# Kernel tuning notes

Hardware: AMD Instinct MI355X
Metric: run time of the kernel (lower is better)

Reference implementation:

```python
import jax, jax.numpy as jnp
from jax import lax
import numpy as np

B, CIN, HC, K, REC = 64, 64, 64, 3, 5
MG = 240 // REC  # 48
EPS = 1e-8


def conv2d(x, w, b, pad):
    y = lax.conv_general_dilated(x, w, (1, 1), [(pad, pad), (pad, pad)],
                                 dimension_numbers=('NCHW', 'OIHW', 'NCHW'))
    return y + b[None, :, None, None]


def conv_transpose2d(x, w, b, stride, pad):
    # PyTorch ConvTranspose2d: w is (Cin, Cout, kH, kW)
    k = w.shape[2]
    w_t = jnp.transpose(w[:, :, ::-1, ::-1], (1, 0, 2, 3))  # -> OIHW, flipped
    y = lax.conv_general_dilated(x, w_t, (1, 1),
                                 [(k - 1 - pad, k - 1 - pad)] * 2,
                                 lhs_dilation=(stride, stride),
                                 dimension_numbers=('NCHW', 'OIHW', 'NCHW'))
    return y + b[None, :, None, None]


def leaky(x):
    return jnp.where(x >= 0, x, 0.2 * x)


def setup_inputs() -> dict:
    key = jax.random.key(0)
    ks = jax.random.split(key, 12)
    s = 0.05
    return {
        'x': jax.random.normal(ks[0], (B, CIN, 64, 64), jnp.float32),
        'h': jax.random.normal(ks[1], (B, HC, 64, 64), jnp.float32),
        'c': jax.random.normal(ks[2], (B, HC, 64, 64), jnp.float32),
        'recalled_memory_feature': jax.random.normal(ks[3], (B, REC, MG, 32, 32), jnp.float32),
        'conv_w': jax.random.normal(ks[4], (5 * HC, CIN + HC, K, K), jnp.float32) * s,
        'conv_b': jax.random.normal(ks[5], (5 * HC,), jnp.float32) * s,
        'convc_w': jax.random.normal(ks[6], (MG, HC, 1, 1), jnp.float32) * s,
        'convc_b': jax.random.normal(ks[7], (MG,), jnp.float32) * s,
        'convssm_w': jax.random.normal(ks[8], (MG, MG, 4, 4), jnp.float32) * s,
        'convssm_b': jax.random.normal(ks[9], (MG,), jnp.float32) * s,
        'convfuse_w': jax.random.normal(ks[10], (HC, MG + HC, 1, 1), jnp.float32) * s,
        'convfuse_b': jax.random.normal(ks[11], (HC,), jnp.float32) * s,
    }


def reference(x, h, c, recalled_memory_feature, conv_w, conv_b, convc_w, convc_b,
              convssm_w, convssm_b, convfuse_w, convfuse_b):
    rm = recalled_memory_feature.reshape(B, REC, MG, 32, 32)
    rm_avg = rm.mean(axis=(3, 4))                      # (B, REC, MG)
    q = leaky(conv2d(c, convc_w, convc_b, 0))          # (B, MG, 64, 64)
    q_avg = q.mean(axis=(2, 3))                        # (B, MG)
    # cosine similarity along channel dim, vectorized over (B, REC)
    qn = jnp.maximum(jnp.linalg.norm(q_avg, axis=1, keepdims=True), EPS)   # (B,1)
    mn = jnp.maximum(jnp.linalg.norm(rm_avg, axis=2), EPS)                  # (B,REC)
    cos = jnp.einsum('bm,brm->br', q_avg, rm_avg) / (qn * mn)               # (B,REC)
    attn = jax.nn.softmax(cos, axis=1)                                      # (B,REC)
    mt = jnp.einsum('br,brmhw->bmhw', attn, rm)        # (B, MG, 32, 32)
    mt = leaky(conv_transpose2d(mt, convssm_w, convssm_b, 2, 1))  # (B, MG, 64, 64)

    gates = conv2d(jnp.concatenate((x, h), axis=1), conv_w, conv_b, K // 2)
    i, f, g, o, lam = jnp.split(gates, 5, axis=1)
    i = jax.nn.sigmoid(i)
    f = jax.nn.sigmoid(f)
    o = jax.nn.sigmoid(o)
    g = jnp.tanh(g)
    lam = jax.nn.sigmoid(lam)
    c_new = f * c + i * g
    h_new = o * jnp.tanh(conv2d(jnp.concatenate((c_new, mt), axis=1), convfuse_w, convfuse_b, 0))
    h_out = lam * h_new + (1.0 - lam) * h
    return (h_out, c_new)
```

## Files before the change

### kernel.cpp

```cpp
#include <hip/hip_runtime.h>
#include <hip/hip_bf16.h>
#include <cstdint>

#define HW 4096
#define MGc 48
#define RECc 5

typedef __attribute__((ext_vector_type(8))) short bf16x8;
typedef __attribute__((ext_vector_type(4))) float f32x4;

__device__ __forceinline__ float sigf(float x) { return 1.f / (1.f + expf(-x)); }
__device__ __forceinline__ float leakyf(float x) { return x >= 0.f ? x : 0.2f * x; }
__device__ __forceinline__ unsigned short f2bfu(float f) {
  __hip_bfloat16 b = __float2bfloat16(f);
  return *reinterpret_cast<unsigned short*>(&b);
}
__device__ __forceinline__ float bfu2f(unsigned short u) {
  unsigned v = ((unsigned)u) << 16;
  return __uint_as_float(v);
}
__device__ __forceinline__ void gload_lds16(const void* g, void* l) {
  __builtin_amdgcn_global_load_lds(
      (const __attribute__((address_space(1))) unsigned int*)g,
      (__attribute__((address_space(3))) unsigned int*)l, 16, 0, 0);
}

__global__ __launch_bounds__(256) void k_prep(const float* __restrict__ cw,
    __hip_bfloat16* __restrict__ Wp, __hip_bfloat16* __restrict__ Pp) {
  if (blockIdx.x < 1440) {
    int idx = blockIdx.x * 256 + threadIdx.x;
    int t = idx / (320 * 128);
    int rem = idx % (320 * 128);
    int ocp = rem / 128, ci = rem % 128;
    int nt = ocp / 80, r2 = ocp % 80, gate = r2 / 16, ml = r2 % 16;
    int oc = gate * 64 + nt * 16 + ml;
    Wp[idx] = __float2bfloat16(cw[((size_t)oc * 128 + ci) * 9 + t]);
  } else {
    int idx = (blockIdx.x - 1440) * 256 + threadIdx.x;
    int b = idx / 4160, i = idx % 4160;
    bf16x8* base = reinterpret_cast<bf16x8*>(Pp);
    size_t u;
    if (i < 2112) {
      int r = (i < 1056) ? 0 : 65;
      int j = (i < 1056) ? i : i - 1056;
      u = ((size_t)b * 66 + r) * 1056 + j;
    } else {
      int i2 = i - 2112;
      int row = 1 + (i2 >> 5), k = i2 & 31;
      int px = (k < 16) ? 0 : 65, ci8 = k & 15;
      u = (((size_t)b * 66 + row) * 66 + px) * 16 + ci8;
    }
    base[u] = (bf16x8)0;
  }
}

__global__ __launch_bounds__(256) void k_rm_sum(const float* __restrict__ rm,
                                                float* __restrict__ rm_sum) {
  int row = blockIdx.x;
  const float4* p = reinterpret_cast<const float4*>(rm + (size_t)row * 1024);
  float4 v = p[threadIdx.x];
  float s = v.x + v.y + v.z + v.w;
  #pragma unroll
  for (int off = 32; off; off >>= 1) s += __shfl_down(s, off);
  __shared__ float sred[4];
  if ((threadIdx.x & 63) == 0) sred[threadIdx.x >> 6] = s;
  __syncthreads();
  if (threadIdx.x == 0) rm_sum[row] = sred[0] + sred[1] + sred[2] + sred[3];
}

__global__ __launch_bounds__(256) void k_q_part(const float* __restrict__ c,
    const float* __restrict__ ccw, const float* __restrict__ ccb,
    float* __restrict__ q_part) {
  __shared__ float wl[MGc * 64];
  __shared__ float bl[MGc];
  __shared__ float red[4][MGc];
  int b = blockIdx.y, seg = blockIdx.x;
  for (int i = threadIdx.x; i < MGc * 64; i += 256) wl[i] = ccw[i];
  if (threadIdx.x < MGc) bl[threadIdx.x] = ccb[threadIdx.x];
  __syncthreads();
  int px = seg * 256 + threadIdx.x;
  float acc[MGc];
  #pragma unroll
  for (int m = 0; m < MGc; m++) acc[m] = 0.f;
  const float* cp = c + (size_t)b * 64 * HW + px;
  for (int ci = 0; ci < 64; ci++) {
    float v = cp[(size_t)ci * HW];
    #pragma unroll
    for (int m = 0; m < MGc; m++) acc[m] += wl[m * 64 + ci] * v;
  }
  int lane = threadIdx.x & 63, wv = threadIdx.x >> 6;
  #pragma unroll
  for (int m = 0; m < MGc; m++) {
    float t = leakyf(acc[m] + bl[m]);
    #pragma unroll
    for (int off = 32; off; off >>= 1) t += __shfl_down(t, off);
    if (lane == 0) red[wv][m] = t;
  }
  __syncthreads();
  if (threadIdx.x < MGc) {
    float t = red[0][threadIdx.x] + red[1][threadIdx.x] + red[2][threadIdx.x] + red[3][threadIdx.x];
    q_part[((size_t)b * 16 + seg) * MGc + threadIdx.x] = t;
  }
}

__global__ __launch_bounds__(256) void k_mt_pre(const float* __restrict__ rm,
    const float* __restrict__ rm_sum, const float* __restrict__ q_part,
    float* __restrict__ mt_pre) {
  __shared__ float sat[RECc];
  int idx = blockIdx.x * 256 + threadIdx.x;
  int b = idx / (MGc * 1024);
  if (threadIdx.x < 64) {
    int lane = threadIdx.x;
    float q = 0.f;
    if (lane < MGc) {
      float s = 0.f;
      for (int sg = 0; sg < 16; sg++) s += q_part[((size_t)b * 16 + sg) * MGc + lane];
      q = s * (1.f / 4096.f);
    }
    float qs = q * q;
    #pragma unroll
    for (int off = 32; off; off >>= 1) qs += __shfl_xor(qs, off);
    float qn = fmaxf(sqrtf(qs), 1e-8f);
    float cosv[RECc];
    #pragma unroll
    for (int r = 0; r < RECc; r++) {
      float m = 0.f;
      if (lane < MGc) m = rm_sum[((size_t)b * RECc + r) * MGc + lane] * (1.f / 1024.f);
      float d = q * m, ms = m * m;
      #pragma unroll
      for (int off = 32; off; off >>= 1) { d += __shfl_xor(d, off); ms += __shfl_xor(ms, off); }
      float mn = fmaxf(sqrtf(ms), 1e-8f);
      cosv[r] = d / (qn * mn);
    }
    float mx = cosv[0];
    #pragma unroll
    for (int r = 1; r < RECc; r++) mx = fmaxf(mx, cosv[r]);
    float ssum = 0.f;
    #pragma unroll
    for (int r = 0; r < RECc; r++) { cosv[r] = expf(cosv[r] - mx); ssum += cosv[r]; }
    float inv = 1.f / ssum;
    #pragma unroll
    for (int r = 0; r < RECc; r++)
      if (lane == r) sat[r] = cosv[r] * inv;
  }
  __syncthreads();
  int rem = idx - b * (MGc * 1024);
  const float* base = rm + (size_t)b * RECc * MGc * 1024 + rem;
  float v = sat[0] * base[0] + sat[1] * base[MGc * 1024] + sat[2] * base[2 * MGc * 1024]
          + sat[3] * base[3 * MGc * 1024] + sat[4] * base[4 * MGc * 1024];
  mt_pre[idx] = v;
}

__global__ __launch_bounds__(512) void k_ssm(const float* __restrict__ mt_pre,
    const float* __restrict__ w, const float* __restrict__ bias,
    __hip_bfloat16* __restrict__ mt) {
  __shared__ float in_t[12][10][20];
  __shared__ float w_t[12][48][16];
  int b = blockIdx.y;
  int tile = blockIdx.x;
  int y0 = (tile >> 1) * 16, x0 = (tile & 1) * 32;
  int wv = threadIdx.x >> 6, lane = threadIdx.x & 63;
  int co0 = wv * 6;
  int oyl = lane >> 2, xseg = lane & 3;
  int oy = y0 + oyl;
  int iy0 = (y0 >> 1) - 1, ix0 = (x0 >> 1) - 1;
  int kyA = (oy + 1) & 1;
  int iyA = (oy + 1 - kyA) >> 1;
  int rA = iyA - iy0, rB = rA - 1;
  float acc[6][8] = {};
  for (int ch = 0; ch < 4; ch++) {
    int ci0 = ch * 12;
    __syncthreads();
    for (int i = threadIdx.x; i < 12 * 10 * 18; i += 512) {
      int ci = i / 180, rr = (i % 180) / 18, cc2 = i % 18;
      int giy = iy0 + rr, gix = ix0 + cc2;
      float v = 0.f;
      if ((unsigned)giy < 32u && (unsigned)gix < 32u)
        v = mt_pre[(((size_t)b * MGc + ci0 + ci) * 32 + giy) * 32 + gix];
      in_t[ci][rr][cc2] = v;
    }
    for (int i = threadIdx.x; i < 12 * 48 * 16; i += 512)
      (&w_t[0][0][0])[i] = w[ci0 * 768 + i];
    __syncthreads();
    #pragma unroll 1
    for (int ci = 0; ci < 12; ci++) {
      float4 a0 = *reinterpret_cast<const float4*>(&in_t[ci][rA][xseg * 4]);
      float4 a1 = *reinterpret_cast<const float4*>(&in_t[ci][rA][xseg * 4 + 4]);
      float4 b0 = *reinterpret_cast<const float4*>(&in_t[ci][rB][xseg * 4]);
      float4 b1 = *reinterpret_cast<const float4*>(&in_t[ci][rB][xseg * 4 + 4]);
      float vA[6] = {a0.x, a0.y, a0.z, a0.w, a1.x, a1.y};
      float vB[6] = {b0.x, b0.y, b0.z, b0.w, b1.x, b1.y};
      #pragma unroll
      for (int co = 0; co < 6; co++) {
        const float* wp = &w_t[ci][co0 + co][0];
        float4 wA = *reinterpret_cast<const float4*>(wp + kyA * 4);
        float4 wB = *reinterpret_cast<const float4*>(wp + (kyA + 2) * 4);
        #pragma unroll
        for (int j = 0; j < 8; j++) {
          if ((j & 1) == 0) {
            int hi = (j >> 1) + 1, lo = j >> 1;
            acc[co][j] += vA[hi] * wA.y + vA[lo] * wA.w + vB[hi] * wB.y + vB[lo] * wB.w;
          } else {
            int hi = ((j + 1) >> 1) + 1, lo = (j + 1) >> 1;
            acc[co][j] += vA[hi] * wA.x + vA[lo] * wA.z + vB[hi] * wB.x + vB[lo] * wB.z;
          }
        }
      }
    }
  }
  int oxb = x0 + xseg * 8;
  #pragma unroll
  for (int co = 0; co < 6; co++) {
    float bb = bias[co0 + co];
    size_t obase = (((size_t)b * MGc + co0 + co) * 64 + oy) * 64 + oxb;
    #pragma unroll
    for (int j = 0; j < 8; j++)
      mt[obase + j] = __float2bfloat16(leakyf(acc[co][j] + bb));
  }
}

__global__ __launch_bounds__(256) void k_ppack(const float* __restrict__ xin,
    const float* __restrict__ hin, __hip_bfloat16* __restrict__ Pp) {
  __shared__ float t[64][65];
  int b = blockIdx.z, y = blockIdx.y, half = blockIdx.x;
  const float* src = (half ? hin : xin) + (size_t)b * 64 * HW + y * 64;
  #pragma unroll
  for (int it = 0; it < 4; it++) {
    int li = it * 256 + threadIdx.x;
    int ci = li >> 4, x4 = (li & 15) * 4;
    float4 v = *reinterpret_cast<const float4*>(src + (size_t)ci * HW + x4);
    t[x4][ci] = v.x; t[x4 + 1][ci] = v.y; t[x4 + 2][ci] = v.z; t[x4 + 3][ci] = v.w;
  }
  __syncthreads();
  int x = threadIdx.x >> 2, c16 = (threadIdx.x & 3) * 16;
  unsigned short* dst = reinterpret_cast<unsigned short*>(Pp) +
      ((((size_t)b * 66 + y + 1) * 66 + x + 1) * 128 + half * 64 + c16);
  bf16x8 o0, o1;
  #pragma unroll
  for (int j = 0; j < 8; j++) {
    o0[j] = (short)f2bfu(t[x][c16 + j]);
    o1[j] = (short)f2bfu(t[x][c16 + 8 + j]);
  }
  *reinterpret_cast<bf16x8*>(dst) = o0;
  *reinterpret_cast<bf16x8*>(dst + 8) = o1;
}

__global__ __launch_bounds__(256) void k_gates_mfma(
    const __hip_bfloat16* __restrict__ Pp, const __hip_bfloat16* __restrict__ Wp,
    const float* __restrict__ c, const float* __restrict__ cb,
    float* __restrict__ c_new, __hip_bfloat16* __restrict__ o_g,
    __hip_bfloat16* __restrict__ lam_g) {
  __shared__ bf16x8 s_in[18 * 4 * 18];
  __shared__ bf16x8 s_w[9 * 4 * 80];
  int orig = blockIdx.y * gridDim.x + blockIdx.x;
  int t_id = (orig & 7) * 512 + (orig >> 3);
  int b = t_id >> 6;
  int r6 = t_id & 63;
  int ytile = r6 >> 4, xtile = (r6 >> 2) & 3, nt = r6 & 3;
  int y0 = ytile * 16, x0 = xtile * 16;
  int tid = threadIdx.x;
  int wv = tid >> 6, lane = tid & 63;
  int lane15 = lane & 15, lq = lane >> 4;

  f32x4 acc[4][5];
  #pragma unroll
  for (int i = 0; i < 4; i++)
    #pragma unroll
    for (int j = 0; j < 5; j++) acc[i][j] = (f32x4)0.f;

  const char* Pb = (const char*)Pp;
  const char* Wb = (const char*)Wp;

  #pragma unroll 1
  for (int cc = 0; cc < 4; cc++) {
    __syncthreads();
    #pragma unroll 1
    for (int u = wv; u < 21; u += 4) {
      int e = u * 64 + lane;
      if (e < 1296) {
        int L = e / 72, r = e - L * 72;
        int llq = r / 18, xi = r - llq * 18;
        const char* gp = Pb + ((((size_t)b * 66 + y0 + L) * 66 + (x0 + xi)) * 256)
                         + cc * 64 + llq * 16;
        gload_lds16(gp, (void*)&s_in[e]);
      }
    }
    #pragma unroll 1
    for (int u = wv; u < 45; u += 4) {
      int e = u * 64 + lane;
      int unit = e / 80, ol = e - unit * 80;
      int t = unit >> 2, g = unit & 3;
      const char* gp = Wb + (((size_t)t * 320 + nt * 80 + ol) * 128 + cc * 32 + g * 8) * 2;
      gload_lds16(gp, (void*)&s_w[e]);
    }
    __syncthreads();

    #pragma unroll
    for (int dx = 0; dx < 3; dx++) {
      #pragma unroll
      for (int ky = 0; ky < 3; ky++) {
        int t = ky * 3 + dx;
        bf16x8 af[4];
        #pragma unroll
        for (int rr = 0; rr < 4; rr++)
          af[rr] = s_in[((wv * 4 + rr + ky) * 4 + lq) * 18 + lane15 + dx];
        bf16x8 bw[5];
        #pragma unroll
        for (int gg = 0; gg < 5; gg++)
          bw[gg] = s_w[(t * 4 + lq) * 80 + gg * 16 + lane15];
        __builtin_amdgcn_s_setprio(1);
        #pragma unroll
        for (int rr = 0; rr < 4; rr++)
          #pragma unroll
          for (int gg = 0; gg < 5; gg++)
            acc[rr][gg] = __builtin_amdgcn_mfma_f32_16x16x32_bf16(
                af[rr], bw[gg], acc[rr][gg], 0, 0, 0);
        __builtin_amdgcn_s_setprio(0);
      }
    }
  }

  int m_hid = nt * 16 + lane15;
  float bi = cb[m_hid], bff = cb[64 + m_hid], bgg = cb[128 + m_hid],
        bo = cb[192 + m_hid], bl = cb[256 + m_hid];
  int xb = x0 + lq * 4;
  size_t chofs = ((size_t)b * 64 + m_hid) * HW;
  #pragma unroll
  for (int rr = 0; rr < 4; rr++) {
    int y = y0 + wv * 4 + rr;
    size_t pofs = chofs + (size_t)y * 64 + xb;
    f32x4 cold = *reinterpret_cast<const f32x4*>(c + pofs);
    f32x4 cn;
    unsigned short ov[4], lv[4];
    #pragma unroll
    for (int e = 0; e < 4; e++) {
      float i_ = sigf(acc[rr][0][e] + bi);
      float f_ = sigf(acc[rr][1][e] + bff);
      float g_ = tanhf(acc[rr][2][e] + bgg);
      float o_ = sigf(acc[rr][3][e] + bo);
      float l_ = sigf(acc[rr][4][e] + bl);
      cn[e] = f_ * cold[e] + i_ * g_;
      ov[e] = f2bfu(o_);
      lv[e] = f2bfu(l_);
    }
    *reinterpret_cast<f32x4*>(c_new + pofs) = cn;
    ushort4 ovv = {ov[0], ov[1], ov[2], ov[3]};
    ushort4 lvv = {lv[0], lv[1], lv[2], lv[3]};
    *reinterpret_cast<ushort4*>(reinterpret_cast<unsigned short*>(o_g) + pofs) = ovv;
    *reinterpret_cast<ushort4*>(reinterpret_cast<unsigned short*>(lam_g) + pofs) = lvv;
  }
}

__global__ __launch_bounds__(256) void k_fuse(const float* __restrict__ c_new,
    const __hip_bfloat16* __restrict__ mt, const __hip_bfloat16* __restrict__ o_g,
    const __hip_bfloat16* __restrict__ lam_g, const float* __restrict__ h,
    const float* __restrict__ fw, const float* __restrict__ fb,
    float* __restrict__ h_out) {
  __shared__ float wl[112][64];
  int b = blockIdx.y, seg = blockIdx.x;
  for (int i = threadIdx.x; i < 112 * 64; i += 256) {
    int ci = i >> 6, co = i & 63;
    wl[ci][co] = fw[co * 112 + ci];
  }
  __syncthreads();
  int px = seg * 512 + threadIdx.x * 2;
  size_t bofs = (size_t)b * 64 * HW;
  float2 acc[64];
  #pragma unroll
  for (int co = 0; co < 64; co++) { float bv = fb[co]; acc[co].x = bv; acc[co].y = bv; }
  #pragma unroll 1
  for (int ci = 0; ci < 64; ci++) {
    float2 v = *reinterpret_cast<const float2*>(c_new + bofs + (size_t)ci * HW + px);
    #pragma unroll
    for (int c4 = 0; c4 < 16; c4++) {
      float4 w = *reinterpret_cast<const float4*>(&wl[ci][c4 * 4]);
      acc[c4 * 4 + 0].x += w.x * v.x; acc[c4 * 4 + 0].y += w.x * v.y;
      acc[c4 * 4 + 1].x += w.y * v.x; acc[c4 * 4 + 1].y += w.y * v.y;
      acc[c4 * 4 + 2].x += w.z * v.x; acc[c4 * 4 + 2].y += w.z * v.y;
      acc[c4 * 4 + 3].x += w.w * v.x; acc[c4 * 4 + 3].y += w.w * v.y;
    }
  }
  const unsigned short* mtu = reinterpret_cast<const unsigned short*>(mt);
  size_t mtofs = (size_t)b * MGc * HW + px;
  #pragma unroll 1
  for (int ci = 0; ci < 48; ci++) {
    unsigned u = *reinterpret_cast<const unsigned*>(mtu + mtofs + (size_t)ci * HW);
    float vx = bfu2f((unsigned short)(u & 0xffff));
    float vy = bfu2f((unsigned short)(u >> 16));
    #pragma unroll
    for (int c4 = 0; c4 < 16; c4++) {
      float4 w = *reinterpret_cast<const float4*>(&wl[64 + ci][c4 * 4]);
      acc[c4 * 4 + 0].x += w.x * vx; acc[c4 * 4 + 0].y += w.x * vy;
      acc[c4 * 4 + 1].x += w.y * vx; acc[c4 * 4 + 1].y += w.y * vy;
      acc[c4 * 4 + 2].x += w.z * vx; acc[c4 * 4 + 2].y += w.z * vy;
      acc[c4 * 4 + 3].x += w.w * vx; acc[c4 * 4 + 3].y += w.w * vy;
    }
  }
  const unsigned short* ou = reinterpret_cast<const unsigned short*>(o_g);
  const unsigned short* lu = reinterpret_cast<const unsigned short*>(lam_g);
  #pragma unroll
  for (int co = 0; co < 64; co++) {
    size_t ofs = bofs + (size_t)co * HW + px;
    unsigned uo = *reinterpret_cast<const unsigned*>(ou + ofs);
    unsigned ul = *reinterpret_cast<const unsigned*>(lu + ofs);
    float2 hv = *reinterpret_cast<const float2*>(h + ofs);
    float hnx = tanhf(acc[co].x), hny = tanhf(acc[co].y);
    float ox = bfu2f((unsigned short)(uo & 0xffff)), oy = bfu2f((unsigned short)(uo >> 16));
    float lx = bfu2f((unsigned short)(ul & 0xffff)), ly = bfu2f((unsigned short)(ul >> 16));
    float2 r;
    r.x = lx * (ox * hnx) + (1.f - lx) * hv.x;
    r.y = ly * (oy * hny) + (1.f - ly) * hv.y;
    *reinterpret_cast<float2*>(h_out + ofs) = r;
  }
}

extern "C" void kernel_launch(void* const* d_in, const int* in_sizes, int n_in,
                              void* d_out, int out_size, void* d_ws, size_t ws_size,
                              hipStream_t stream) {
  const float* x   = (const float*)d_in[0];
  const float* h   = (const float*)d_in[1];
  const float* c   = (const float*)d_in[2];
  const float* rm  = (const float*)d_in[3];
  const float* cw  = (const float*)d_in[4];
  const float* cb  = (const float*)d_in[5];
  const float* ccw = (const float*)d_in[6];
  const float* ccb = (const float*)d_in[7];
  const float* sw  = (const float*)d_in[8];
  const float* sb  = (const float*)d_in[9];
  const float* fw  = (const float*)d_in[10];
  const float* fb  = (const float*)d_in[11];

  float* h_out = (float*)d_out;
  float* c_new = h_out + (size_t)16777216;

  char* ws = (char*)d_ws;
  float* rm_sum = (float*)(ws + 0);
  float* q_part = (float*)(ws + 65536);
  float* mt_pre = (float*)(ws + 262144);
  __hip_bfloat16* o_g   = (__hip_bfloat16*)(ws + 0);
  __hip_bfloat16* lam_g = (__hip_bfloat16*)(ws + 33554432);
  __hip_bfloat16* mt    = (__hip_bfloat16*)(ws + 67108864);
  __hip_bfloat16* Pp    = (__hip_bfloat16*)(ws + 92274688);
  __hip_bfloat16* Wp    = (__hip_bfloat16*)(ws + 163643392);

  k_prep<<<2480, 256, 0, stream>>>(cw, Wp, Pp);
  k_ppack<<<dim3(2, 64, 64), 256, 0, stream>>>(x, h, Pp);
  k_rm_sum<<<15360, 256, 0, stream>>>(rm, rm_sum);
  k_q_part<<<dim3(16, 64), 256, 0, stream>>>(c, ccw, ccb, q_part);
  k_mt_pre<<<12288, 256, 0, stream>>>(rm, rm_sum, q_part, mt_pre);
  k_ssm<<<dim3(8, 64), 512, 0, stream>>>(mt_pre, sw, sb, mt);
  k_gates_mfma<<<dim3(64, 64), 256, 0, stream>>>(Pp, Wp, c, cb, c_new, o_g, lam_g);
  k_fuse<<<dim3(8, 64), 256, 0, stream>>>(c_new, mt, o_g, lam_g, h, fw, fb, h_out);
}
```

Before: 637.1 us.

## Merge four prologue kernels into one launch and hoist gate-kernel load addressing

Four independent prologue kernels (weight prep and padding zeroing, input packing, memory row sums, query partial sums) are merged into one launch that dispatches on block index, cutting launch count and letting the phases overlap on the GPU. In the gates MFMA kernel, the global-to-LDS copy addresses are computed once before the channel-chunk loop instead of in every iteration. The A-fragment loads from LDS are also restructured so six rows are loaded once per dx and reused across the three ky taps. The merged kernel reserves the largest shared-memory footprint for every block, which can lower occupancy for the small-footprint branches. The gates kernel now holds more registers for the precomputed pointers and extra fragments.

```diff
diff --git a/kernel.cpp b/kernel.cpp
--- a/kernel.cpp
+++ b/kernel.cpp
@@ -25,18 +25,25 @@
       (__attribute__((address_space(3))) unsigned int*)l, 16, 0, 0);
 }
 
-__global__ __launch_bounds__(256) void k_prep(const float* __restrict__ cw,
-    __hip_bfloat16* __restrict__ Wp, __hip_bfloat16* __restrict__ Pp) {
-  if (blockIdx.x < 1440) {
-    int idx = blockIdx.x * 256 + threadIdx.x;
+__global__ __launch_bounds__(256) void k_head(const float* __restrict__ cw,
+    __hip_bfloat16* __restrict__ Wp, __hip_bfloat16* __restrict__ Pp,
+    const float* __restrict__ xin, const float* __restrict__ hin,
+    const float* __restrict__ rm, float* __restrict__ rm_sum,
+    const float* __restrict__ c, const float* __restrict__ ccw,
+    const float* __restrict__ ccb, float* __restrict__ q_part) {
+  __shared__ __align__(16) char smem[16704];
+  int bid = blockIdx.x;
+  int tid = threadIdx.x;
+  if (bid < 1440) {
+    int idx = bid * 256 + tid;
     int t = idx / (320 * 128);
     int rem = idx % (320 * 128);
     int ocp = rem / 128, ci = rem % 128;
     int nt = ocp / 80, r2 = ocp % 80, gate = r2 / 16, ml = r2 % 16;
     int oc = gate * 64 + nt * 16 + ml;
     Wp[idx] = __float2bfloat16(cw[((size_t)oc * 128 + ci) * 9 + t]);
-  } else {
-    int idx = (blockIdx.x - 1440) * 256 + threadIdx.x;
+  } else if (bid < 2480) {
+    int idx = (bid - 1440) * 256 + tid;
     int b = idx / 4160, i = idx % 4160;
     bf16x8* base = reinterpret_cast<bf16x8*>(Pp);
     size_t u;
@@ -51,55 +58,73 @@
       u = (((size_t)b * 66 + row) * 66 + px) * 16 + ci8;
     }
     base[u] = (bf16x8)0;
-  }
-}
-
-__global__ __launch_bounds__(256) void k_rm_sum(const float* __restrict__ rm,
-                                                float* __restrict__ rm_sum) {
-  int row = blockIdx.x;
-  const float4* p = reinterpret_cast<const float4*>(rm + (size_t)row * 1024);
-  float4 v = p[threadIdx.x];
-  float s = v.x + v.y + v.z + v.w;
-  #pragma unroll
-  for (int off = 32; off; off >>= 1) s += __shfl_down(s, off);
-  __shared__ float sred[4];
-  if ((threadIdx.x & 63) == 0) sred[threadIdx.x >> 6] = s;
-  __syncthreads();
-  if (threadIdx.x == 0) rm_sum[row] = sred[0] + sred[1] + sred[2] + sred[3];
-}
-
-__global__ __launch_bounds__(256) void k_q_part(const float* __restrict__ c,
-    const float* __restrict__ ccw, const float* __restrict__ ccb,
-    float* __restrict__ q_part) {
-  __shared__ float wl[MGc * 64];
-  __shared__ float bl[MGc];
-  __shared__ float red[4][MGc];
-  int b = blockIdx.y, seg = blockIdx.x;
-  for (int i = threadIdx.x; i < MGc * 64; i += 256) wl[i] = ccw[i];
-  if (threadIdx.x < MGc) bl[threadIdx.x] = ccb[threadIdx.x];
-  __syncthreads();
-  int px = seg * 256 + threadIdx.x;
-  float acc[MGc];
-  #pragma unroll
-  for (int m = 0; m < MGc; m++) acc[m] = 0.f;
-  const float* cp = c + (size_t)b * 64 * HW + px;
-  for (int ci = 0; ci < 64; ci++) {
-    float v = cp[(size_t)ci * HW];
-    #pragma unroll
-    for (int m = 0; m < MGc; m++) acc[m] += wl[m * 64 + ci] * v;
-  }
-  int lane = threadIdx.x & 63, wv = threadIdx.x >> 6;
-  #pragma unroll
-  for (int m = 0; m < MGc; m++) {
-    float t = leakyf(acc[m] + bl[m]);
-    #pragma unroll
-    for (int off = 32; off; off >>= 1) t += __shfl_down(t, off);
-    if (lane == 0) red[wv][m] = t;
-  }
-  __syncthreads();
-  if (threadIdx.x < MGc) {
-    float t = red[0][threadIdx.x] + red[1][threadIdx.x] + red[2][threadIdx.x] + red[3][threadIdx.x];
-    q_part[((size_t)b * 16 + seg) * MGc + threadIdx.x] = t;
+  } else if (bid < 10672) {
+    float (*t)[65] = (float(*)[65])smem;
+    int r = bid - 2480;
+    int half = r & 1, y = (r >> 1) & 63, b = r >> 7;
+    const float* src = (half ? hin : xin) + (size_t)b * 64 * HW + y * 64;
+    #pragma unroll
+    for (int it = 0; it < 4; it++) {
+      int li = it * 256 + tid;
+      int ci = li >> 4, x4 = (li & 15) * 4;
+      float4 v = *reinterpret_cast<const float4*>(src + (size_t)ci * HW + x4);
+      t[x4][ci] = v.x; t[x4 + 1][ci] = v.y; t[x4 + 2][ci] = v.z; t[x4 + 3][ci] = v.w;
+    }
+    __syncthreads();
+    int x = tid >> 2, c16 = (tid & 3) * 16;
+    unsigned short* dst = reinterpret_cast<unsigned short*>(Pp) +
+        ((((size_t)b * 66 + y + 1) * 66 + x + 1) * 128 + half * 64 + c16);
+    bf16x8 o0, o1;
+    #pragma unroll
+    for (int j = 0; j < 8; j++) {
+      o0[j] = (short)f2bfu(t[x][c16 + j]);
+      o1[j] = (short)f2bfu(t[x][c16 + 8 + j]);
+    }
+    *reinterpret_cast<bf16x8*>(dst) = o0;
+    *reinterpret_cast<bf16x8*>(dst + 8) = o1;
+  } else if (bid < 26032) {
+    float* sred = (float*)smem;
+    int row = bid - 10672;
+    const float4* p = reinterpret_cast<const float4*>(rm + (size_t)row * 1024);
+    float4 v = p[tid];
+    float s = v.x + v.y + v.z + v.w;
+    #pragma unroll
+    for (int off = 32; off; off >>= 1) s += __shfl_down(s, off);
+    if ((tid & 63) == 0) sred[tid >> 6] = s;
+    __syncthreads();
+    if (tid == 0) rm_sum[row] = sred[0] + sred[1] + sred[2] + sred[3];
+  } else {
+    float* wl = (float*)smem;
+    float* bl = wl + MGc * 64;
+    float (*red)[MGc] = (float(*)[MGc])(bl + 64);
+    int r = bid - 26032;
+    int seg = r & 15, b = r >> 4;
+    for (int i = tid; i < MGc * 64; i += 256) wl[i] = ccw[i];
+    if (tid < MGc) bl[tid] = ccb[tid];
+    __syncthreads();
+    int px = seg * 256 + tid;
+    float acc[MGc];
+    #pragma unroll
+    for (int m = 0; m < MGc; m++) acc[m] = 0.f;
+    const float* cp = c + (size_t)b * 64 * HW + px;
+    for (int ci = 0; ci < 64; ci++) {
+      float v = cp[(size_t)ci * HW];
+      #pragma unroll
+      for (int m = 0; m < MGc; m++) acc[m] += wl[m * 64 + ci] * v;
+    }
+    int lane = tid & 63, wv = tid >> 6;
+    #pragma unroll
+    for (int m = 0; m < MGc; m++) {
+      float t2 = leakyf(acc[m] + bl[m]);
+      #pragma unroll
+      for (int off = 32; off; off >>= 1) t2 += __shfl_down(t2, off);
+      if (lane == 0) red[wv][m] = t2;
+    }
+    __syncthreads();
+    if (tid < MGc) {
+      float t2 = red[0][tid] + red[1][tid] + red[2][tid] + red[3][tid];
+      q_part[((size_t)b * 16 + seg) * MGc + tid] = t2;
+    }
   }
 }
 
@@ -219,32 +244,6 @@
   }
 }
 
-__global__ __launch_bounds__(256) void k_ppack(const float* __restrict__ xin,
-    const float* __restrict__ hin, __hip_bfloat16* __restrict__ Pp) {
-  __shared__ float t[64][65];
-  int b = blockIdx.z, y = blockIdx.y, half = blockIdx.x;
-  const float* src = (half ? hin : xin) + (size_t)b * 64 * HW + y * 64;
-  #pragma unroll
-  for (int it = 0; it < 4; it++) {
-    int li = it * 256 + threadIdx.x;
-    int ci = li >> 4, x4 = (li & 15) * 4;
-    float4 v = *reinterpret_cast<const float4*>(src + (size_t)ci * HW + x4);
-    t[x4][ci] = v.x; t[x4 + 1][ci] = v.y; t[x4 + 2][ci] = v.z; t[x4 + 3][ci] = v.w;
-  }
-  __syncthreads();
-  int x = threadIdx.x >> 2, c16 = (threadIdx.x & 3) * 16;
-  unsigned short* dst = reinterpret_cast<unsigned short*>(Pp) +
-      ((((size_t)b * 66 + y + 1) * 66 + x + 1) * 128 + half * 64 + c16);
-  bf16x8 o0, o1;
-  #pragma unroll
-  for (int j = 0; j < 8; j++) {
-    o0[j] = (short)f2bfu(t[x][c16 + j]);
-    o1[j] = (short)f2bfu(t[x][c16 + 8 + j]);
-  }
-  *reinterpret_cast<bf16x8*>(dst) = o0;
-  *reinterpret_cast<bf16x8*>(dst + 8) = o1;
-}
-
 __global__ __launch_bounds__(256) void k_gates_mfma(
     const __hip_bfloat16* __restrict__ Pp, const __hip_bfloat16* __restrict__ Wp,
     const float* __restrict__ c, const float* __restrict__ cb,
@@ -262,48 +261,61 @@
   int wv = tid >> 6, lane = tid & 63;
   int lane15 = lane & 15, lq = lane >> 4;
 
-  f32x4 acc[4][5];
-  #pragma unroll
-  for (int i = 0; i < 4; i++)
-    #pragma unroll
-    for (int j = 0; j < 5; j++) acc[i][j] = (f32x4)0.f;
-
   const char* Pb = (const char*)Pp;
   const char* Wb = (const char*)Wp;
 
+  const char* gin[6]; int din[6]; bool ain[6];
+  #pragma unroll
+  for (int k = 0; k < 6; k++) {
+    int u = wv + 4 * k;
+    int e = u * 64 + lane;
+    ain[k] = (u < 21) && (e < 1296);
+    int ee = (e < 1296) ? e : 0;
+    int L = ee / 72, r = ee - L * 72;
+    int llq = r / 18, xi = r - llq * 18;
+    gin[k] = Pb + ((((size_t)b * 66 + y0 + L) * 66 + (x0 + xi)) * 256) + llq * 16;
+    din[k] = ee;
+  }
+  const char* gw[12]; int dw[12]; bool aw[12];
+  #pragma unroll
+  for (int k = 0; k < 12; k++) {
+    int u = wv + 4 * k;
+    aw[k] = (u < 45);
+    int uu = (u < 45) ? u : 0;
+    int e = uu * 64 + lane;
+    int unit = e / 80, ol = e - unit * 80;
+    int t = unit >> 2, g = unit & 3;
+    gw[k] = Wb + (((size_t)t * 320 + nt * 80 + ol) * 128 + g * 8) * 2;
+    dw[k] = e;
+  }
+
+  f32x4 acc[4][5];
+  #pragma unroll
+  for (int i = 0; i < 4; i++)
+    #pragma unroll
+    for (int j = 0; j < 5; j++) acc[i][j] = (f32x4)0.f;
+
   #pragma unroll 1
   for (int cc = 0; cc < 4; cc++) {
     __syncthreads();
-    #pragma unroll 1
-    for (int u = wv; u < 21; u += 4) {
-      int e = u * 64 + lane;
-      if (e < 1296) {
-        int L = e / 72, r = e - L * 72;
-        int llq = r / 18, xi = r - llq * 18;
-        const char* gp = Pb + ((((size_t)b * 66 + y0 + L) * 66 + (x0 + xi)) * 256)
-                         + cc * 64 + llq * 16;
-        gload_lds16(gp, (void*)&s_in[e]);
-      }
-    }
-    #pragma unroll 1
-    for (int u = wv; u < 45; u += 4) {
-      int e = u * 64 + lane;
-      int unit = e / 80, ol = e - unit * 80;
-      int t = unit >> 2, g = unit & 3;
-      const char* gp = Wb + (((size_t)t * 320 + nt * 80 + ol) * 128 + cc * 32 + g * 8) * 2;
-      gload_lds16(gp, (void*)&s_w[e]);
-    }
+    int co = cc * 64;
+    #pragma unroll
+    for (int k = 0; k < 6; k++)
+      if (ain[k]) gload_lds16(gin[k] + co, (void*)&s_in[din[k]]);
+    #pragma unroll
+    for (int k = 0; k < 12; k++)
+      if (aw[k]) gload_lds16(gw[k] + co, (void*)&s_w[dw[k]]);
     __syncthreads();
 
     #pragma unroll
     for (int dx = 0; dx < 3; dx++) {
+      bf16x8 af[6];
+      #pragma unroll
+      for (int r = 0; r < 6; r++)
+        af[r] = s_in[((wv * 4 + r) * 4 + lq) * 18 + lane15 + dx];
       #pragma unroll
       for (int ky = 0; ky < 3; ky++) {
         int t = ky * 3 + dx;
-        bf16x8 af[4];
-        #pragma unroll
-        for (int rr = 0; rr < 4; rr++)
-          af[rr] = s_in[((wv * 4 + rr + ky) * 4 + lq) * 18 + lane15 + dx];
         bf16x8 bw[5];
         #pragma unroll
         for (int gg = 0; gg < 5; gg++)
@@ -314,7 +326,7 @@
           #pragma unroll
           for (int gg = 0; gg < 5; gg++)
             acc[rr][gg] = __builtin_amdgcn_mfma_f32_16x16x32_bf16(
-                af[rr], bw[gg], acc[rr][gg], 0, 0, 0);
+                af[rr + ky], bw[gg], acc[rr][gg], 0, 0, 0);
         __builtin_amdgcn_s_setprio(0);
       }
     }
@@ -443,10 +455,7 @@
   __hip_bfloat16* Pp    = (__hip_bfloat16*)(ws + 92274688);
   __hip_bfloat16* Wp    = (__hip_bfloat16*)(ws + 163643392);
 
-  k_prep<<<2480, 256, 0, stream>>>(cw, Wp, Pp);
-  k_ppack<<<dim3(2, 64, 64), 256, 0, stream>>>(x, h, Pp);
-  k_rm_sum<<<15360, 256, 0, stream>>>(rm, rm_sum);
-  k_q_part<<<dim3(16, 64), 256, 0, stream>>>(c, ccw, ccb, q_part);
+  k_head<<<27056, 256, 0, stream>>>(cw, Wp, Pp, x, h, rm, rm_sum, c, ccw, ccb, q_part);
   k_mt_pre<<<12288, 256, 0, stream>>>(rm, rm_sum, q_part, mt_pre);
   k_ssm<<<dim3(8, 64), 512, 0, stream>>>(mt_pre, sw, sb, mt);
   k_gates_mfma<<<dim3(64, 64), 256, 0, stream>>>(Pp, Wp, c, cb, c_new, o_g, lam_g);
```

Result: slower. 655.9 us (+3.0%).
